# Optimization experiments

Measured on AMD Instinct MI355X. Metric: run time of the kernel, lower is better.

The kernel has to match this reference:

```python
import jax, jax.numpy as jnp
import numpy as np

H = 64           # edge/node/global hidden size
IN_F = 4         # node_attr_size
OUT_F = 1        # out_size
NUM_EMB = 100    # edge_num_embeddings
SKIP = True


def setup_inputs() -> dict:
    key = jax.random.key(0)
    ks = jax.random.split(key, 24)
    T, N, E = 4, 20000, 320000
    NNZ = 340000
    inp = {
        'node_attr': jax.random.normal(ks[0], (T, N, IN_F), jnp.float32),
        'global_attr': jax.random.normal(ks[1], (1, H), jnp.float32),
        'L_values': jax.random.normal(ks[2], (NNZ,), jnp.float32),
        'coeff': jnp.ones((1,), jnp.float32),
        'edge_attr': jax.random.randint(ks[3], (T, E), 0, NUM_EMB),
        'edge_index': jax.random.randint(ks[4], (2, E), 0, N),
        'L_index': jax.random.randint(ks[5], (2, NNZ), 0, N),
        'num_processing_steps': 4,
        # parameters
        'emb': jax.random.normal(ks[6], (NUM_EMB, H), jnp.float32) * 0.05,
        'W_ne': jax.random.normal(ks[7], (IN_F, H), jnp.float32) * 0.1,
        'b_ne': jnp.zeros((H,), jnp.float32),
        'W_eb': jax.random.normal(ks[8], ((H + 2 * H) * 2 + H, H), jnp.float32) * 0.05,
        'b_eb': jnp.zeros((H,), jnp.float32),
        'W_nb': jax.random.normal(ks[9], (2 * H + 2 * H + H, H), jnp.float32) * 0.05,
        'b_nb': jnp.zeros((H,), jnp.float32),
        'W_gb': jax.random.normal(ks[10], (H + H + H, H), jnp.float32) * 0.05,
        'b_gb': jnp.zeros((H,), jnp.float32),
        'W_d1': jax.random.normal(ks[11], (H, H), jnp.float32) * 0.1,
        'b_d1': jnp.zeros((H,), jnp.float32),
        'W_d2': jax.random.normal(ks[12], (H, OUT_F), jnp.float32) * 0.1,
        'b_d2': jnp.zeros((OUT_F,), jnp.float32),
        'W_i1': jax.random.normal(ks[13], (H, H), jnp.float32) * 0.1,
        'b_i1': jnp.zeros((H,), jnp.float32),
        'W_i2': jax.random.normal(ks[14], (H, IN_F), jnp.float32) * 0.1,
        'b_i2': jnp.zeros((IN_F,), jnp.float32),
    }
    return inp


def reference(node_attr, global_attr, L_values, coeff, emb, W_ne, b_ne,
              W_eb, b_eb, W_nb, b_nb, W_gb, b_gb, W_d1, b_d1, W_d2, b_d2,
              W_i1, b_i1, W_i2, b_i2, edge_attr, edge_index, L_index,
              num_processing_steps):
    T, N, _ = node_attr.shape
    s, r = edge_index[0], edge_index[1]
    Li, Lj = L_index[0], L_index[1]

    # encoders (all T steps at once)
    x_enc = jax.nn.relu(node_attr @ W_ne + b_ne)   # [T,N,H]
    e_enc = emb[edge_attr]                         # [T,E,H]

    def laplacian(h):  # sparse sp_L @ h, h: [N,H]
        return jax.ops.segment_sum(L_values[:, None] * h[Lj], Li, num_segments=N)

    def step(carry, xe):
        h_x, h_e, h_g = carry
        x_t, e_t = xe
        node_cat = jnp.concatenate([x_t, h_x], axis=-1)          # [N,2H]
        edge_cat = jnp.concatenate([e_t, h_e], axis=-1)          # [E,2H]
        g = h_g[0]                                               # [H]
        E_ = edge_cat.shape[0]
        # EdgeBlock: edges + sender + receiver + globals
        eb_in = jnp.concatenate([edge_cat, node_cat[s], node_cat[r],
                                 jnp.broadcast_to(g, (E_, g.shape[0]))], axis=-1)
        e_new = jax.nn.relu(eb_in @ W_eb + b_eb)                 # [E,H]
        # NodeBlock: scatter_add aggregates of received/sent edges
        recv = jax.ops.segment_sum(e_new, r, num_segments=N)
        sent = jax.ops.segment_sum(e_new, s, num_segments=N)
        nb_in = jnp.concatenate([recv, sent, node_cat,
                                 jnp.broadcast_to(g, (N, g.shape[0]))], axis=-1)
        x_new = jax.nn.relu(nb_in @ W_nb + b_nb)                 # [N,H]
        # GlobalBlock: scatter_mean (single graph -> mean)
        gb_in = jnp.concatenate([e_new.mean(0), x_new.mean(0), g])[None]
        g_new = jax.nn.relu(gb_in @ W_gb + b_gb)                 # [1,H]
        h_x_next = h_x + x_new if SKIP else x_new
        time_d = h_x_next - h_x
        spat_d = coeff[0] * laplacian(h_x_next)  # pde='diff': coeff * L u
        return (h_x_next, e_new, g_new), (h_x_next, time_d, spat_d)

    h0 = (jnp.zeros((N, H), jnp.float32),
          jnp.zeros((e_enc.shape[1], H), jnp.float32),
          global_attr)
    _, (hid, time_d, spat_d) = jax.lax.scan(step, h0, (x_enc, e_enc))

    # decoders over all steps
    out_nodes = jax.nn.relu(hid @ W_d1 + b_d1) @ W_d2 + b_d2     # [T,N,OUT_F]
    pred_in = jax.nn.relu(hid @ W_i1 + b_i1) @ W_i2 + b_i2       # [T,N,IN_F]
    return out_nodes, time_d, spat_d, pred_in
```

## Files before the change

kernel.cpp:

```cpp
#include <hip/hip_runtime.h>

#define TT 4
#define NN 20000
#define EE 320000
#define NZ 340000

typedef __attribute__((ext_vector_type(8))) __bf16 bf16x8;
typedef __attribute__((ext_vector_type(16))) float f32x16;

__device__ __forceinline__ unsigned short f2bf(float f) {
    unsigned int u = __float_as_uint(f);
    u = (u + 0x7FFFu + ((u >> 16) & 1u)) >> 16;
    return (unsigned short)u;
}
__device__ __forceinline__ float bf2f(unsigned short h) {
    return __uint_as_float(((unsigned int)h) << 16);
}

#define GLL16(src, dst) __builtin_amdgcn_global_load_lds( \
    (const __attribute__((address_space(1))) unsigned int*)(src), \
    (__attribute__((address_space(3))) unsigned int*)(dst), 16, 0, 0)

__global__ void k_count(const int* __restrict__ r, const int* __restrict__ s,
                        const int* __restrict__ Li,
                        int* cnt_r, int* cnt_s, int* cnt_L) {
    int i = blockIdx.x * 256 + threadIdx.x;
    if (i < EE) { atomicAdd(&cnt_r[r[i]], 1); atomicAdd(&cnt_s[s[i]], 1); }
    if (i < NZ) { atomicAdd(&cnt_L[Li[i]], 1); }
}

__global__ __launch_bounds__(1024) void k_scan(int* cnt, int* rowp, int* wp) {
    int which = blockIdx.x;
    int* c = cnt + which * NN;
    int* row = rowp + which * (NN + 1);
    int* w = wp + which * NN;
    __shared__ int ssum[1024];
    int tid = threadIdx.x;
    const int CH = (NN + 1023) / 1024;
    int base = tid * CH;
    int s = 0;
    for (int i = 0; i < CH; ++i) { int idx = base + i; s += (idx < NN) ? c[idx] : 0; }
    ssum[tid] = s;
    __syncthreads();
    for (int o = 1; o < 1024; o <<= 1) {
        int v = (tid >= o) ? ssum[tid - o] : 0;
        __syncthreads();
        ssum[tid] += v;
        __syncthreads();
    }
    int run = (tid > 0) ? ssum[tid - 1] : 0;
    for (int i = 0; i < CH; ++i) {
        int idx = base + i;
        if (idx < NN) { row[idx] = run; w[idx] = run; run += c[idx]; }
    }
    if (tid == 1023) row[NN] = ssum[1023];
}

__global__ void k_scatter(const int* __restrict__ r, const int* __restrict__ s,
                          const int* __restrict__ Li, const int* __restrict__ Lj,
                          const float* __restrict__ Lv,
                          int* wp_r, int* wp_s, int* wp_L,
                          int* col_r, int* col_s, int* col_Lj, float* col_Lv) {
    int i = blockIdx.x * 256 + threadIdx.x;
    if (i < EE) {
        col_r[atomicAdd(&wp_r[r[i]], 1)] = i;
        col_s[atomicAdd(&wp_s[s[i]], 1)] = i;
    }
    if (i < NZ) {
        int pos = atomicAdd(&wp_L[Li[i]], 1);
        col_Lj[pos] = Lj[i];
        col_Lv[pos] = Lv[i];
    }
}

__global__ __launch_bounds__(256) void k_pack(
    const float* __restrict__ W_eb, const float* __restrict__ W_nb,
    const float* __restrict__ W_d1, const float* __restrict__ W_i1,
    const float* __restrict__ emb, unsigned short* __restrict__ Bpe,
    unsigned short* __restrict__ Bpn, unsigned short* __restrict__ Bpd,
    unsigned short* __restrict__ emb_bf) {
    int t = blockIdx.x * 256 + threadIdx.x;
    if (t < 2 * 24 * 512) {
        int i = t & 7, l = (t >> 3) & 63, kb = (t >> 9) % 24, ch = t / (24 * 512);
        int colv = ch * 32 + (l & 31);
        int k = kb * 16 + (l >> 5) * 8 + i;
        Bpe[t] = f2bf(W_eb[k * 64 + colv]);
    }
    if (t < 2 * 16 * 512) {
        int i = t & 7, l = (t >> 3) & 63, kb = (t >> 9) % 16, ch = t / (16 * 512);
        int colv = ch * 32 + (l & 31);
        int k = kb * 16 + (l >> 5) * 8 + i;
        Bpn[t] = f2bf(W_nb[k * 64 + colv]);
    }
    if (t < 4 * 4 * 512) {
        int i = t & 7, l = (t >> 3) & 63, kb = (t >> 9) & 3, sec = t >> 11;
        int colv = (sec & 1) * 32 + (l & 31);
        int k = kb * 16 + (l >> 5) * 8 + i;
        const float* W = (sec < 2) ? W_d1 : W_i1;
        Bpd[t] = f2bf(W[k * 64 + colv]);
    }
    if (t < 100 * 64) emb_bf[t] = f2bf(emb[t]);
}

__global__ __launch_bounds__(256) void k_xenc(const float* __restrict__ na,
                                              const float* __restrict__ W_ne,
                                              const float* __restrict__ b_ne,
                                              unsigned short* __restrict__ xenc) {
    int row = blockIdx.x * 4 + (threadIdx.x >> 6);
    int j = threadIdx.x & 63;
    float4 a = *(const float4*)&na[(size_t)row * 4];
    float v = b_ne[j] + a.x * W_ne[j] + a.y * W_ne[64 + j] + a.z * W_ne[128 + j] + a.w * W_ne[192 + j];
    xenc[(size_t)row * 64 + j] = f2bf(fmaxf(v, 0.f));
}

__global__ void k_gbias(int do_update, const float* __restrict__ W_gb,
                        const float* __restrict__ b_gb, const float* __restrict__ W_eb,
                        const float* __restrict__ b_eb, const float* __restrict__ W_nb,
                        const float* __restrict__ b_nb, float* __restrict__ g_cur,
                        float* __restrict__ e_sum, float* __restrict__ x_sum,
                        float* __restrict__ gb_eb, float* __restrict__ gb_nb) {
    int j = threadIdx.x;
    float a = 0.f;
    if (do_update) {
        a = b_gb[j];
        for (int k = 0; k < 64; ++k) a += (e_sum[k] / (float)EE) * W_gb[k * 64 + j];
        for (int k = 0; k < 64; ++k) a += (x_sum[k] / (float)NN) * W_gb[(64 + k) * 64 + j];
        for (int k = 0; k < 64; ++k) a += g_cur[k] * W_gb[(128 + k) * 64 + j];
    }
    __syncthreads();
    if (do_update) {
        g_cur[j] = fmaxf(a, 0.f);
        e_sum[j] = 0.f;
        x_sum[j] = 0.f;
    }
    __syncthreads();
    float a1 = b_eb[j], a2 = b_nb[j];
    for (int k = 0; k < 64; ++k) {
        float gk = g_cur[k];
        a1 = fmaf(gk, W_eb[(384 + k) * 64 + j], a1);
        a2 = fmaf(gk, W_nb[(256 + k) * 64 + j], a2);
    }
    gb_eb[j] = a1;
    gb_nb[j] = a2;
}

__global__ __launch_bounds__(512) void k_edge(
    const unsigned short* __restrict__ xenc_t, unsigned short* __restrict__ h_e,
    const unsigned short* __restrict__ hx_bf, const unsigned short* __restrict__ emb_bf,
    const int* __restrict__ eattr_t, const int* __restrict__ sidx,
    const int* __restrict__ ridx, const unsigned short* __restrict__ Bp,
    const float* __restrict__ gbias, float* __restrict__ e_sum) {
    __shared__ unsigned short sBe[24576];
    __shared__ float sRed[8][64];
    const int tid = threadIdx.x;
    const int w = tid >> 6, ln = tid & 63;
    const int er = ln & 31, hi = ln >> 5;
    const int ebase = blockIdx.x * 256 + w * 32;
    const int e = ebase + er;
    const int si = sidx[e], ri = ridx[e], ai = eattr_t[e];

    #pragma unroll
    for (int i = 0; i < 6; ++i) {
        int off = i * 4096 + w * 512;
        GLL16(Bp + off + ln * 8, sBe + off);
    }

    const unsigned short* base0 = emb_bf + (size_t)64 * ai + hi * 8;
    const unsigned short* base1 = h_e + (size_t)64 * e + hi * 8;
    const unsigned short* base2 = xenc_t + (size_t)64 * si + hi * 8;
    const unsigned short* base3 = hx_bf + (size_t)64 * si + hi * 8;
    const unsigned short* base4 = xenc_t + (size_t)64 * ri + hi * 8;
    const unsigned short* base5 = hx_bf + (size_t)64 * ri + hi * 8;
    const unsigned short* bases[6] = {base0, base1, base2, base3, base4, base5};

    f32x16 acc0, acc1;
    #pragma unroll
    for (int i = 0; i < 16; ++i) { acc0[i] = 0.f; acc1[i] = 0.f; }

    bf16x8 c0 = *(const bf16x8*)(base0);
    bf16x8 c1 = *(const bf16x8*)(base0 + 16);
    bf16x8 c2 = *(const bf16x8*)(base0 + 32);
    bf16x8 c3 = *(const bf16x8*)(base0 + 48);

    __syncthreads();

    #pragma unroll
    for (int c = 0; c < 6; ++c) {
        bf16x8 n0, n1, n2, n3;
        if (c < 5) {
            const unsigned short* nb = bases[c + 1];
            n0 = *(const bf16x8*)(nb);
            n1 = *(const bf16x8*)(nb + 16);
            n2 = *(const bf16x8*)(nb + 32);
            n3 = *(const bf16x8*)(nb + 48);
        }
        {
            bf16x8 b0 = *(const bf16x8*)&sBe[((c * 4 + 0) * 64 + ln) * 8];
            bf16x8 b1 = *(const bf16x8*)&sBe[((24 + c * 4 + 0) * 64 + ln) * 8];
            acc0 = __builtin_amdgcn_mfma_f32_32x32x16_bf16(c0, b0, acc0, 0, 0, 0);
            acc1 = __builtin_amdgcn_mfma_f32_32x32x16_bf16(c0, b1, acc1, 0, 0, 0);
            b0 = *(const bf16x8*)&sBe[((c * 4 + 1) * 64 + ln) * 8];
            b1 = *(const bf16x8*)&sBe[((24 + c * 4 + 1) * 64 + ln) * 8];
            acc0 = __builtin_amdgcn_mfma_f32_32x32x16_bf16(c1, b0, acc0, 0, 0, 0);
            acc1 = __builtin_amdgcn_mfma_f32_32x32x16_bf16(c1, b1, acc1, 0, 0, 0);
            b0 = *(const bf16x8*)&sBe[((c * 4 + 2) * 64 + ln) * 8];
            b1 = *(const bf16x8*)&sBe[((24 + c * 4 + 2) * 64 + ln) * 8];
            acc0 = __builtin_amdgcn_mfma_f32_32x32x16_bf16(c2, b0, acc0, 0, 0, 0);
            acc1 = __builtin_amdgcn_mfma_f32_32x32x16_bf16(c2, b1, acc1, 0, 0, 0);
            b0 = *(const bf16x8*)&sBe[((c * 4 + 3) * 64 + ln) * 8];
            b1 = *(const bf16x8*)&sBe[((24 + c * 4 + 3) * 64 + ln) * 8];
            acc0 = __builtin_amdgcn_mfma_f32_32x32x16_bf16(c3, b0, acc0, 0, 0, 0);
            acc1 = __builtin_amdgcn_mfma_f32_32x32x16_bf16(c3, b1, acc1, 0, 0, 0);
        }
        c0 = n0; c1 = n1; c2 = n2; c3 = n3;
    }

    const float gb0 = gbias[er], gb1 = gbias[er + 32];
    float cs0 = 0.f, cs1 = 0.f;
    #pragma unroll
    for (int r = 0; r < 16; ++r) {
        int row = (r & 3) + 8 * (r >> 2) + 4 * hi;
        size_t o = (size_t)(ebase + row) * 64;
        float v0 = fmaxf(acc0[r] + gb0, 0.f);
        float v1 = fmaxf(acc1[r] + gb1, 0.f);
        cs0 += v0; cs1 += v1;
        h_e[o + er] = f2bf(v0);
        h_e[o + er + 32] = f2bf(v1);
    }
    cs0 += __shfl_xor(cs0, 32, 64);
    cs1 += __shfl_xor(cs1, 32, 64);
    if (hi == 0) { sRed[w][er] = cs0; sRed[w][er + 32] = cs1; }
    __syncthreads();
    if (w == 0) {
        float t = 0.f;
        #pragma unroll
        for (int q = 0; q < 8; ++q) t += sRed[q][ln];
        atomicAdd(&e_sum[ln], t);
    }
}

__global__ __launch_bounds__(256) void k_gather(
    const unsigned short* __restrict__ h_e, const int* __restrict__ row_r,
    const int* __restrict__ col_r, const int* __restrict__ row_s,
    const int* __restrict__ col_s, unsigned short* __restrict__ recv,
    unsigned short* __restrict__ sentb) {
    int t = blockIdx.x * 256 + threadIdx.x;
    int g = t & 15, n = t >> 4;
    float a0, a1, a2, a3;
    uint2 packed;

    a0 = a1 = a2 = a3 = 0.f;
    int b0 = row_r[n], b1 = row_r[n + 1];
    for (int p = b0; p < b1; ++p) {
        uint2 v = *(const uint2*)&h_e[(size_t)64 * col_r[p] + g * 4];
        a0 += bf2f((unsigned short)(v.x & 0xFFFF));
        a1 += bf2f((unsigned short)(v.x >> 16));
        a2 += bf2f((unsigned short)(v.y & 0xFFFF));
        a3 += bf2f((unsigned short)(v.y >> 16));
    }
    packed.x = (unsigned int)f2bf(a0) | ((unsigned int)f2bf(a1) << 16);
    packed.y = (unsigned int)f2bf(a2) | ((unsigned int)f2bf(a3) << 16);
    *(uint2*)&recv[(size_t)64 * n + g * 4] = packed;

    a0 = a1 = a2 = a3 = 0.f;
    b0 = row_s[n]; b1 = row_s[n + 1];
    for (int p = b0; p < b1; ++p) {
        uint2 v = *(const uint2*)&h_e[(size_t)64 * col_s[p] + g * 4];
        a0 += bf2f((unsigned short)(v.x & 0xFFFF));
        a1 += bf2f((unsigned short)(v.x >> 16));
        a2 += bf2f((unsigned short)(v.y & 0xFFFF));
        a3 += bf2f((unsigned short)(v.y >> 16));
    }
    packed.x = (unsigned int)f2bf(a0) | ((unsigned int)f2bf(a1) << 16);
    packed.y = (unsigned int)f2bf(a2) | ((unsigned int)f2bf(a3) << 16);
    *(uint2*)&sentb[(size_t)64 * n + g * 4] = packed;
}

#define NODE_CHUNK(CIDX, BASE)                                                          \
    {                                                                                   \
        const unsigned short* src = (BASE) + hi * 8;                                    \
        _Pragma("unroll") for (int kb = 0; kb < 4; ++kb) {                              \
            bf16x8 a = *(const bf16x8*)(src + kb * 16);                                 \
            bf16x8 b0 = *(const bf16x8*)&Bp[(size_t)(((CIDX)*4 + kb) * 64 + ln) * 8];   \
            bf16x8 b1 = *(const bf16x8*)&Bp[(size_t)((16 + (CIDX)*4 + kb) * 64 + ln) * 8]; \
            acc0 = __builtin_amdgcn_mfma_f32_32x32x16_bf16(a, b0, acc0, 0, 0, 0);       \
            acc1 = __builtin_amdgcn_mfma_f32_32x32x16_bf16(a, b1, acc1, 0, 0, 0);       \
        }                                                                               \
    }

__global__ __launch_bounds__(64) void k_node(
    const unsigned short* __restrict__ recv, const unsigned short* __restrict__ sentb,
    const unsigned short* __restrict__ xenc_t, float* __restrict__ h_x,
    unsigned short* __restrict__ hx_bf, const unsigned short* __restrict__ Bp,
    const float* __restrict__ gbias, float* __restrict__ x_sum,
    unsigned short* __restrict__ hid_t, float* __restrict__ timed_t) {
    const int ln = threadIdx.x;
    const int er = ln & 31, hi = ln >> 5;
    const int n0 = blockIdx.x * 32;
    const int n = n0 + er;

    f32x16 acc0, acc1;
    #pragma unroll
    for (int i = 0; i < 16; ++i) { acc0[i] = 0.f; acc1[i] = 0.f; }

    NODE_CHUNK(0, recv + (size_t)64 * n)
    NODE_CHUNK(1, sentb + (size_t)64 * n)
    NODE_CHUNK(2, xenc_t + (size_t)64 * n)
    NODE_CHUNK(3, hx_bf + (size_t)64 * n)

    const float gb0 = gbias[er], gb1 = gbias[er + 32];
    float cs0 = 0.f, cs1 = 0.f;
    #pragma unroll
    for (int r = 0; r < 16; ++r) {
        int row = (r & 3) + 8 * (r >> 2) + 4 * hi;
        size_t o = (size_t)(n0 + row) * 64;
        float x0 = fmaxf(acc0[r] + gb0, 0.f);
        float x1 = fmaxf(acc1[r] + gb1, 0.f);
        cs0 += x0; cs1 += x1;
        float hx0 = h_x[o + er] + x0;
        float hx1 = h_x[o + er + 32] + x1;
        unsigned short hb0 = f2bf(hx0), hb1 = f2bf(hx1);
        h_x[o + er] = hx0;        h_x[o + er + 32] = hx1;
        hx_bf[o + er] = hb0;      hx_bf[o + er + 32] = hb1;
        hid_t[o + er] = hb0;      hid_t[o + er + 32] = hb1;
        timed_t[o + er] = x0;     timed_t[o + er + 32] = x1;
    }
    cs0 += __shfl_xor(cs0, 32, 64);
    cs1 += __shfl_xor(cs1, 32, 64);
    if (hi == 0) {
        atomicAdd(&x_sum[er], cs0);
        atomicAdd(&x_sum[er + 32], cs1);
    }
}

__global__ __launch_bounds__(256) void k_lap(
    const float* __restrict__ h_x, const int* __restrict__ row_L,
    const int* __restrict__ col_Lj, const float* __restrict__ col_Lv,
    const float* __restrict__ coeff, float* __restrict__ spat_t) {
    int t = blockIdx.x * 256 + threadIdx.x;
    int g = t & 15, n = t >> 4;
    float a0 = 0.f, a1 = 0.f, a2 = 0.f, a3 = 0.f;
    int b0 = row_L[n], b1 = row_L[n + 1];
    for (int p = b0; p < b1; ++p) {
        float lv = col_Lv[p];
        int j = col_Lj[p];
        float4 v = *(const float4*)&h_x[(size_t)64 * j + g * 4];
        a0 = fmaf(lv, v.x, a0);
        a1 = fmaf(lv, v.y, a1);
        a2 = fmaf(lv, v.z, a2);
        a3 = fmaf(lv, v.w, a3);
    }
    float c = coeff[0];
    float4 outv = {c * a0, c * a1, c * a2, c * a3};
    *(float4*)&spat_t[(size_t)64 * n + g * 4] = outv;
}

__global__ __launch_bounds__(256) void k_dec(
    const unsigned short* __restrict__ hid_bf, const unsigned short* __restrict__ Bpd,
    const float* __restrict__ b_d1, const float* __restrict__ W_d2,
    const float* __restrict__ b_d2, const float* __restrict__ b_i1,
    const float* __restrict__ W_i2, const float* __restrict__ b_i2,
    float* __restrict__ out_nodes, float* __restrict__ pred_in) {
    __shared__ unsigned short sDec[4][32 * 138];
    const int tid = threadIdx.x;
    const int w = tid >> 6, ln = tid & 63;
    const int er = ln & 31, hi = ln >> 5;
    const int row0 = (blockIdx.x * 4 + w) * 32;

    f32x16 ad0, ad1, ai0, ai1;
    #pragma unroll
    for (int i = 0; i < 16; ++i) { ad0[i] = 0.f; ad1[i] = 0.f; ai0[i] = 0.f; ai1[i] = 0.f; }

    const unsigned short* src = hid_bf + (size_t)(row0 + er) * 64 + hi * 8;
    #pragma unroll
    for (int kb = 0; kb < 4; ++kb) {
        bf16x8 a = *(const bf16x8*)(src + kb * 16);
        bf16x8 bd0 = *(const bf16x8*)&Bpd[((0 * 4 + kb) * 64 + ln) * 8];
        bf16x8 bd1 = *(const bf16x8*)&Bpd[((4 + kb) * 64 + ln) * 8];
        bf16x8 bi0 = *(const bf16x8*)&Bpd[((8 + kb) * 64 + ln) * 8];
        bf16x8 bi1 = *(const bf16x8*)&Bpd[((12 + kb) * 64 + ln) * 8];
        ad0 = __builtin_amdgcn_mfma_f32_32x32x16_bf16(a, bd0, ad0, 0, 0, 0);
        ad1 = __builtin_amdgcn_mfma_f32_32x32x16_bf16(a, bd1, ad1, 0, 0, 0);
        ai0 = __builtin_amdgcn_mfma_f32_32x32x16_bf16(a, bi0, ai0, 0, 0, 0);
        ai1 = __builtin_amdgcn_mfma_f32_32x32x16_bf16(a, bi1, ai1, 0, 0, 0);
    }

    const float bd0v = b_d1[er], bd1v = b_d1[er + 32];
    const float bi0v = b_i1[er], bi1v = b_i1[er + 32];
    unsigned short* sw = &sDec[w][0];
    #pragma unroll
    for (int r = 0; r < 16; ++r) {
        int row = (r & 3) + 8 * (r >> 2) + 4 * hi;
        sw[row * 138 + er]       = f2bf(fmaxf(ad0[r] + bd0v, 0.f));
        sw[row * 138 + er + 32]  = f2bf(fmaxf(ad1[r] + bd1v, 0.f));
        sw[row * 138 + er + 64]  = f2bf(fmaxf(ai0[r] + bi0v, 0.f));
        sw[row * 138 + er + 96]  = f2bf(fmaxf(ai1[r] + bi1v, 0.f));
    }
    __syncthreads();

    const int g_row = row0 + er;
    if (hi == 0) {
        float s = 0.f;
        for (int k = 0; k < 32; ++k) {
            unsigned int u = *(const unsigned int*)&sw[er * 138 + 2 * k];
            s = fmaf(bf2f((unsigned short)(u & 0xFFFF)), W_d2[2 * k], s);
            s = fmaf(bf2f((unsigned short)(u >> 16)), W_d2[2 * k + 1], s);
        }
        out_nodes[g_row] = s + b_d2[0];
    } else {
        float s0 = 0.f, s1 = 0.f, s2 = 0.f, s3 = 0.f;
        for (int k = 0; k < 32; ++k) {
            unsigned int u = *(const unsigned int*)&sw[er * 138 + 64 + 2 * k];
            float vlo = bf2f((unsigned short)(u & 0xFFFF));
            float vhi = bf2f((unsigned short)(u >> 16));
            float4 w0 = *(const float4*)&W_i2[(2 * k) * 4];
            float4 w1 = *(const float4*)&W_i2[(2 * k + 1) * 4];
            s0 = fmaf(vlo, w0.x, fmaf(vhi, w1.x, s0));
            s1 = fmaf(vlo, w0.y, fmaf(vhi, w1.y, s1));
            s2 = fmaf(vlo, w0.z, fmaf(vhi, w1.z, s2));
            s3 = fmaf(vlo, w0.w, fmaf(vhi, w1.w, s3));
        }
        float4 pv = {s0 + b_i2[0], s1 + b_i2[1], s2 + b_i2[2], s3 + b_i2[3]};
        *(float4*)&pred_in[(size_t)4 * g_row] = pv;
    }
}

extern "C" void kernel_launch(void* const* d_in, const int* in_sizes, int n_in,
                              void* d_out, int out_size, void* d_ws, size_t ws_size,
                              hipStream_t stream) {
    (void)in_sizes; (void)n_in; (void)out_size; (void)ws_size;
    const float* node_attr   = (const float*)d_in[0];
    const float* global_attr = (const float*)d_in[1];
    const float* L_values    = (const float*)d_in[2];
    const float* coeff       = (const float*)d_in[3];
    const int*   edge_attr   = (const int*)d_in[4];
    const int*   edge_index  = (const int*)d_in[5];
    const int*   L_index     = (const int*)d_in[6];
    const float* emb  = (const float*)d_in[8];
    const float* W_ne = (const float*)d_in[9];
    const float* b_ne = (const float*)d_in[10];
    const float* W_eb = (const float*)d_in[11];
    const float* b_eb = (const float*)d_in[12];
    const float* W_nb = (const float*)d_in[13];
    const float* b_nb = (const float*)d_in[14];
    const float* W_gb = (const float*)d_in[15];
    const float* b_gb = (const float*)d_in[16];
    const float* W_d1 = (const float*)d_in[17];
    const float* b_d1 = (const float*)d_in[18];
    const float* W_d2 = (const float*)d_in[19];
    const float* b_d2 = (const float*)d_in[20];
    const float* W_i1 = (const float*)d_in[21];
    const float* b_i1 = (const float*)d_in[22];
    const float* W_i2 = (const float*)d_in[23];
    const float* b_i2 = (const float*)d_in[24];

    const int* s_idx = edge_index;
    const int* r_idx = edge_index + EE;
    const int* Li = L_index;
    const int* Lj = L_index + NZ;

    char* ws = (char*)d_ws;
    size_t off = 0;
    auto alloc = [&](size_t bytes) -> void* {
        void* p = ws + off;
        off = (off + bytes + 255) & ~(size_t)255;
        return p;
    };
    unsigned short* xenc   = (unsigned short*)alloc((size_t)TT * NN * 64 * 2);
    unsigned short* hid    = (unsigned short*)alloc((size_t)TT * NN * 64 * 2);
    float*          h_x    = (float*)alloc((size_t)NN * 64 * 4);
    unsigned short* hx_bf  = (unsigned short*)alloc((size_t)NN * 64 * 2);
    unsigned short* h_e    = (unsigned short*)alloc((size_t)EE * 64 * 2);
    unsigned short* recv   = (unsigned short*)alloc((size_t)NN * 64 * 2);
    unsigned short* sentb  = (unsigned short*)alloc((size_t)NN * 64 * 2);
    float* smalls          = (float*)alloc(2048);
    unsigned short* Bpe    = (unsigned short*)alloc((size_t)2 * 24 * 512 * 2);
    unsigned short* Bpn    = (unsigned short*)alloc((size_t)2 * 16 * 512 * 2);
    unsigned short* Bpd    = (unsigned short*)alloc((size_t)4 * 4 * 512 * 2);
    unsigned short* emb_bf = (unsigned short*)alloc((size_t)100 * 64 * 2);
    int* cnt    = (int*)alloc((size_t)3 * NN * 4);
    int* rowp   = (int*)alloc((size_t)3 * (NN + 1) * 4);
    int* wp     = (int*)alloc((size_t)3 * NN * 4);
    int* col_r  = (int*)alloc((size_t)EE * 4);
    int* col_s  = (int*)alloc((size_t)EE * 4);
    int* col_Lj = (int*)alloc((size_t)NZ * 4);
    float* col_Lv = (float*)alloc((size_t)NZ * 4);

    float* g_cur = smalls;
    float* e_sum = smalls + 64;
    float* x_sum = smalls + 128;
    float* gb_eb = smalls + 192;
    float* gb_nb = smalls + 256;
    int* cnt_r = cnt, *cnt_s = cnt + NN, *cnt_L = cnt + 2 * NN;
    int* row_r = rowp, *row_s = rowp + (NN + 1), *row_L = rowp + 2 * (NN + 1);
    int* wp_r = wp, *wp_s = wp + NN, *wp_L = wp + 2 * NN;

    float* out_nodes = (float*)d_out;
    float* time_d = out_nodes + (size_t)TT * NN;
    float* spat_d = time_d + (size_t)TT * NN * 64;
    float* pred_in = spat_d + (size_t)TT * NN * 64;

    hipMemsetAsync(h_x, 0, (size_t)NN * 64 * 4, stream);
    hipMemsetAsync(hx_bf, 0, (size_t)NN * 64 * 2, stream);
    hipMemsetAsync(h_e, 0, (size_t)EE * 64 * 2, stream);
    hipMemsetAsync(smalls, 0, 2048, stream);
    hipMemsetAsync(cnt, 0, (size_t)3 * NN * 4, stream);
    hipMemcpyAsync(g_cur, global_attr, 64 * 4, hipMemcpyDeviceToDevice, stream);

    k_count<<<(NZ + 255) / 256, 256, 0, stream>>>(r_idx, s_idx, Li, cnt_r, cnt_s, cnt_L);
    k_scan<<<3, 1024, 0, stream>>>(cnt, rowp, wp);
    k_scatter<<<(NZ + 255) / 256, 256, 0, stream>>>(r_idx, s_idx, Li, Lj, L_values,
                                                    wp_r, wp_s, wp_L,
                                                    col_r, col_s, col_Lj, col_Lv);
    k_pack<<<96, 256, 0, stream>>>(W_eb, W_nb, W_d1, W_i1, emb, Bpe, Bpn, Bpd, emb_bf);
    k_xenc<<<TT * NN / 4, 256, 0, stream>>>(node_attr, W_ne, b_ne, xenc);
    k_gbias<<<1, 64, 0, stream>>>(0, W_gb, b_gb, W_eb, b_eb, W_nb, b_nb,
                                  g_cur, e_sum, x_sum, gb_eb, gb_nb);

    for (int t = 0; t < TT; ++t) {
        const unsigned short* xenc_t = xenc + (size_t)t * NN * 64;
        k_edge<<<EE / 256, 512, 0, stream>>>(xenc_t, h_e, hx_bf, emb_bf,
                                             edge_attr + (size_t)t * EE, s_idx, r_idx,
                                             Bpe, gb_eb, e_sum);
        k_gather<<<NN * 16 / 256, 256, 0, stream>>>(h_e, row_r, col_r, row_s, col_s,
                                                    recv, sentb);
        k_node<<<NN / 32, 64, 0, stream>>>(recv, sentb, xenc_t, h_x, hx_bf,
                                           Bpn, gb_nb, x_sum,
                                           hid + (size_t)t * NN * 64,
                                           time_d + (size_t)t * NN * 64);
        k_lap<<<NN * 16 / 256, 256, 0, stream>>>(h_x, row_L, col_Lj, col_Lv, coeff,
                                                 spat_d + (size_t)t * NN * 64);
        k_gbias<<<1, 64, 0, stream>>>(1, W_gb, b_gb, W_eb, b_eb, W_nb, b_nb,
                                      g_cur, e_sum, x_sum, gb_eb, gb_nb);
    }
    k_dec<<<TT * NN / 128, 256, 0, stream>>>(hid, Bpd, b_d1, W_d2, b_d2,
                                             b_i1, W_i2, b_i2, out_nodes, pred_in);
}
```

Measured before the change: 761.8 us.

## Precompute per-node sender/receiver edge projections and split gather/laplacian work across threads

```diff
diff --git a/kernel.cpp b/kernel.cpp
--- a/kernel.cpp
+++ b/kernel.cpp
@@ -60,7 +60,7 @@
                           const int* __restrict__ Li, const int* __restrict__ Lj,
                           const float* __restrict__ Lv,
                           int* wp_r, int* wp_s, int* wp_L,
-                          int* col_r, int* col_s, int* col_Lj, float* col_Lv) {
+                          int* col_r, int* col_s, uint2* col_L8) {
     int i = blockIdx.x * 256 + threadIdx.x;
     if (i < EE) {
         col_r[atomicAdd(&wp_r[r[i]], 1)] = i;
@@ -68,8 +68,10 @@
     }
     if (i < NZ) {
         int pos = atomicAdd(&wp_L[Li[i]], 1);
-        col_Lj[pos] = Lj[i];
-        col_Lv[pos] = Lv[i];
+        uint2 v;
+        v.x = (unsigned int)Lj[i];
+        v.y = __float_as_uint(Lv[i]);
+        col_L8[pos] = v;
     }
 }
 
@@ -77,14 +79,20 @@
     const float* __restrict__ W_eb, const float* __restrict__ W_nb,
     const float* __restrict__ W_d1, const float* __restrict__ W_i1,
     const float* __restrict__ emb, unsigned short* __restrict__ Bpe,
-    unsigned short* __restrict__ Bpn, unsigned short* __restrict__ Bpd,
-    unsigned short* __restrict__ emb_bf) {
+    unsigned short* __restrict__ Bpu, unsigned short* __restrict__ Bpn,
+    unsigned short* __restrict__ Bpd, unsigned short* __restrict__ emb_bf) {
     int t = blockIdx.x * 256 + threadIdx.x;
-    if (t < 2 * 24 * 512) {
-        int i = t & 7, l = (t >> 3) & 63, kb = (t >> 9) % 24, ch = t / (24 * 512);
+    if (t < 2 * 8 * 512) {
+        int i = t & 7, l = (t >> 3) & 63, kb = (t >> 9) & 7, ch = t >> 12;
         int colv = ch * 32 + (l & 31);
         int k = kb * 16 + (l >> 5) * 8 + i;
         Bpe[t] = f2bf(W_eb[k * 64 + colv]);
+    }
+    if (t < 4 * 8 * 512) {
+        int i = t & 7, l = (t >> 3) & 63, kb = (t >> 9) & 7, g = t >> 12;
+        int colv = (g & 1) * 32 + (l & 31);
+        int k = 128 + (g >> 1) * 128 + kb * 16 + (l >> 5) * 8 + i;
+        Bpu[t] = f2bf(W_eb[k * 64 + colv]);
     }
     if (t < 2 * 16 * 512) {
         int i = t & 7, l = (t >> 3) & 63, kb = (t >> 9) % 16, ch = t / (16 * 512);
@@ -144,85 +152,112 @@
     gb_nb[j] = a2;
 }
 
+__global__ __launch_bounds__(64) void k_usr(
+    const unsigned short* __restrict__ xenc_t, const unsigned short* __restrict__ hx_bf,
+    const unsigned short* __restrict__ Bpu, float2* __restrict__ usr) {
+    const int ln = threadIdx.x;
+    const int er = ln & 31, hi = ln >> 5;
+    const int n0 = blockIdx.x * 32;
+    const int n = n0 + er;
+
+    f32x16 a0, a1, a2, a3;
+    #pragma unroll
+    for (int i = 0; i < 16; ++i) { a0[i] = 0.f; a1[i] = 0.f; a2[i] = 0.f; a3[i] = 0.f; }
+
+    const unsigned short* sx = xenc_t + (size_t)64 * n + hi * 8;
+    const unsigned short* sh = hx_bf + (size_t)64 * n + hi * 8;
+    #pragma unroll
+    for (int c = 0; c < 2; ++c) {
+        const unsigned short* src = c ? sh : sx;
+        #pragma unroll
+        for (int kb = 0; kb < 4; ++kb) {
+            bf16x8 a = *(const bf16x8*)(src + kb * 16);
+            int kg = c * 4 + kb;
+            bf16x8 b0 = *(const bf16x8*)&Bpu[(size_t)((0 * 8 + kg) * 64 + ln) * 8];
+            bf16x8 b1 = *(const bf16x8*)&Bpu[(size_t)((1 * 8 + kg) * 64 + ln) * 8];
+            bf16x8 b2 = *(const bf16x8*)&Bpu[(size_t)((2 * 8 + kg) * 64 + ln) * 8];
+            bf16x8 b3 = *(const bf16x8*)&Bpu[(size_t)((3 * 8 + kg) * 64 + ln) * 8];
+            a0 = __builtin_amdgcn_mfma_f32_32x32x16_bf16(a, b0, a0, 0, 0, 0);
+            a1 = __builtin_amdgcn_mfma_f32_32x32x16_bf16(a, b1, a1, 0, 0, 0);
+            a2 = __builtin_amdgcn_mfma_f32_32x32x16_bf16(a, b2, a2, 0, 0, 0);
+            a3 = __builtin_amdgcn_mfma_f32_32x32x16_bf16(a, b3, a3, 0, 0, 0);
+        }
+    }
+    #pragma unroll
+    for (int r = 0; r < 16; ++r) {
+        int row = (r & 3) + 8 * (r >> 2) + 4 * hi;
+        size_t o = (size_t)(n0 + row) * 64;
+        float2 vs = {a0[r], a1[r]};
+        float2 vr = {a2[r], a3[r]};
+        usr[o + er] = vs;
+        usr[o + 32 + er] = vr;
+    }
+}
+
 __global__ __launch_bounds__(512) void k_edge(
-    const unsigned short* __restrict__ xenc_t, unsigned short* __restrict__ h_e,
-    const unsigned short* __restrict__ hx_bf, const unsigned short* __restrict__ emb_bf,
-    const int* __restrict__ eattr_t, const int* __restrict__ sidx,
-    const int* __restrict__ ridx, const unsigned short* __restrict__ Bp,
-    const float* __restrict__ gbias, float* __restrict__ e_sum) {
-    __shared__ unsigned short sBe[24576];
+    unsigned short* __restrict__ h_e, const unsigned short* __restrict__ emb_bf,
+    const float2* __restrict__ usr, const int* __restrict__ eattr_t,
+    const int* __restrict__ sidx, const int* __restrict__ ridx,
+    const unsigned short* __restrict__ Bp, const float* __restrict__ gbias,
+    float* __restrict__ e_sum) {
+    __shared__ unsigned short sBe[8192];
     __shared__ float sRed[8][64];
     const int tid = threadIdx.x;
     const int w = tid >> 6, ln = tid & 63;
     const int er = ln & 31, hi = ln >> 5;
     const int ebase = blockIdx.x * 256 + w * 32;
     const int e = ebase + er;
-    const int si = sidx[e], ri = ridx[e], ai = eattr_t[e];
-
-    #pragma unroll
-    for (int i = 0; i < 6; ++i) {
+
+    const int siv = sidx[ebase + er];
+    const int riv = ridx[ebase + er];
+    const int ai = eattr_t[e];
+
+    #pragma unroll
+    for (int i = 0; i < 2; ++i) {
         int off = i * 4096 + w * 512;
         GLL16(Bp + off + ln * 8, sBe + off);
     }
 
-    const unsigned short* base0 = emb_bf + (size_t)64 * ai + hi * 8;
-    const unsigned short* base1 = h_e + (size_t)64 * e + hi * 8;
-    const unsigned short* base2 = xenc_t + (size_t)64 * si + hi * 8;
-    const unsigned short* base3 = hx_bf + (size_t)64 * si + hi * 8;
-    const unsigned short* base4 = xenc_t + (size_t)64 * ri + hi * 8;
-    const unsigned short* base5 = hx_bf + (size_t)64 * ri + hi * 8;
-    const unsigned short* bases[6] = {base0, base1, base2, base3, base4, base5};
+    const unsigned short* s0 = emb_bf + (size_t)64 * ai + hi * 8;
+    const unsigned short* s1 = h_e + (size_t)64 * e + hi * 8;
+    bf16x8 a0 = *(const bf16x8*)(s0);
+    bf16x8 a1 = *(const bf16x8*)(s0 + 16);
+    bf16x8 a2 = *(const bf16x8*)(s0 + 32);
+    bf16x8 a3 = *(const bf16x8*)(s0 + 48);
+    bf16x8 a4 = *(const bf16x8*)(s1);
+    bf16x8 a5 = *(const bf16x8*)(s1 + 16);
+    bf16x8 a6 = *(const bf16x8*)(s1 + 32);
+    bf16x8 a7 = *(const bf16x8*)(s1 + 48);
 
     f32x16 acc0, acc1;
     #pragma unroll
     for (int i = 0; i < 16; ++i) { acc0[i] = 0.f; acc1[i] = 0.f; }
 
-    bf16x8 c0 = *(const bf16x8*)(base0);
-    bf16x8 c1 = *(const bf16x8*)(base0 + 16);
-    bf16x8 c2 = *(const bf16x8*)(base0 + 32);
-    bf16x8 c3 = *(const bf16x8*)(base0 + 48);
-
     __syncthreads();
 
-    #pragma unroll
-    for (int c = 0; c < 6; ++c) {
-        bf16x8 n0, n1, n2, n3;
-        if (c < 5) {
-            const unsigned short* nb = bases[c + 1];
-            n0 = *(const bf16x8*)(nb);
-            n1 = *(const bf16x8*)(nb + 16);
-            n2 = *(const bf16x8*)(nb + 32);
-            n3 = *(const bf16x8*)(nb + 48);
+    #define EMM(AF, KG)                                                              \
+        {                                                                            \
+            bf16x8 b0 = *(const bf16x8*)&sBe[(((KG)) * 64 + ln) * 8];                \
+            bf16x8 b1 = *(const bf16x8*)&sBe[((8 + (KG)) * 64 + ln) * 8];            \
+            acc0 = __builtin_amdgcn_mfma_f32_32x32x16_bf16(AF, b0, acc0, 0, 0, 0);   \
+            acc1 = __builtin_amdgcn_mfma_f32_32x32x16_bf16(AF, b1, acc1, 0, 0, 0);   \
         }
-        {
-            bf16x8 b0 = *(const bf16x8*)&sBe[((c * 4 + 0) * 64 + ln) * 8];
-            bf16x8 b1 = *(const bf16x8*)&sBe[((24 + c * 4 + 0) * 64 + ln) * 8];
-            acc0 = __builtin_amdgcn_mfma_f32_32x32x16_bf16(c0, b0, acc0, 0, 0, 0);
-            acc1 = __builtin_amdgcn_mfma_f32_32x32x16_bf16(c0, b1, acc1, 0, 0, 0);
-            b0 = *(const bf16x8*)&sBe[((c * 4 + 1) * 64 + ln) * 8];
-            b1 = *(const bf16x8*)&sBe[((24 + c * 4 + 1) * 64 + ln) * 8];
-            acc0 = __builtin_amdgcn_mfma_f32_32x32x16_bf16(c1, b0, acc0, 0, 0, 0);
-            acc1 = __builtin_amdgcn_mfma_f32_32x32x16_bf16(c1, b1, acc1, 0, 0, 0);
-            b0 = *(const bf16x8*)&sBe[((c * 4 + 2) * 64 + ln) * 8];
-            b1 = *(const bf16x8*)&sBe[((24 + c * 4 + 2) * 64 + ln) * 8];
-            acc0 = __builtin_amdgcn_mfma_f32_32x32x16_bf16(c2, b0, acc0, 0, 0, 0);
-            acc1 = __builtin_amdgcn_mfma_f32_32x32x16_bf16(c2, b1, acc1, 0, 0, 0);
-            b0 = *(const bf16x8*)&sBe[((c * 4 + 3) * 64 + ln) * 8];
-            b1 = *(const bf16x8*)&sBe[((24 + c * 4 + 3) * 64 + ln) * 8];
-            acc0 = __builtin_amdgcn_mfma_f32_32x32x16_bf16(c3, b0, acc0, 0, 0, 0);
-            acc1 = __builtin_amdgcn_mfma_f32_32x32x16_bf16(c3, b1, acc1, 0, 0, 0);
-        }
-        c0 = n0; c1 = n1; c2 = n2; c3 = n3;
-    }
+    EMM(a0, 0) EMM(a1, 1) EMM(a2, 2) EMM(a3, 3)
+    EMM(a4, 4) EMM(a5, 5) EMM(a6, 6) EMM(a7, 7)
+    #undef EMM
 
     const float gb0 = gbias[er], gb1 = gbias[er + 32];
     float cs0 = 0.f, cs1 = 0.f;
     #pragma unroll
     for (int r = 0; r < 16; ++r) {
         int row = (r & 3) + 8 * (r >> 2) + 4 * hi;
+        int si_row = __shfl(siv, row, 64);
+        int ri_row = __shfl(riv, row, 64);
+        float2 us = usr[(size_t)si_row * 64 + er];
+        float2 ur = usr[(size_t)ri_row * 64 + 32 + er];
         size_t o = (size_t)(ebase + row) * 64;
-        float v0 = fmaxf(acc0[r] + gb0, 0.f);
-        float v1 = fmaxf(acc1[r] + gb1, 0.f);
+        float v0 = fmaxf(acc0[r] + us.x + ur.x + gb0, 0.f);
+        float v1 = fmaxf(acc1[r] + us.y + ur.y + gb1, 0.f);
         cs0 += v0; cs1 += v1;
         h_e[o + er] = f2bf(v0);
         h_e[o + er + 32] = f2bf(v1);
@@ -245,35 +280,25 @@
     const int* __restrict__ col_s, unsigned short* __restrict__ recv,
     unsigned short* __restrict__ sentb) {
     int t = blockIdx.x * 256 + threadIdx.x;
-    int g = t & 15, n = t >> 4;
-    float a0, a1, a2, a3;
-    uint2 packed;
-
-    a0 = a1 = a2 = a3 = 0.f;
-    int b0 = row_r[n], b1 = row_r[n + 1];
+    int sub = t & 31, n = t >> 5;
+    int g = sub & 15, which = sub >> 4;
+    const int* rowp = which ? row_s : row_r;
+    const int* colp = which ? col_s : col_r;
+    unsigned short* outp = which ? sentb : recv;
+
+    float a0 = 0.f, a1 = 0.f, a2 = 0.f, a3 = 0.f;
+    int b0 = rowp[n], b1 = rowp[n + 1];
     for (int p = b0; p < b1; ++p) {
-        uint2 v = *(const uint2*)&h_e[(size_t)64 * col_r[p] + g * 4];
+        uint2 v = *(const uint2*)&h_e[(size_t)64 * colp[p] + g * 4];
         a0 += bf2f((unsigned short)(v.x & 0xFFFF));
         a1 += bf2f((unsigned short)(v.x >> 16));
         a2 += bf2f((unsigned short)(v.y & 0xFFFF));
         a3 += bf2f((unsigned short)(v.y >> 16));
     }
+    uint2 packed;
     packed.x = (unsigned int)f2bf(a0) | ((unsigned int)f2bf(a1) << 16);
     packed.y = (unsigned int)f2bf(a2) | ((unsigned int)f2bf(a3) << 16);
-    *(uint2*)&recv[(size_t)64 * n + g * 4] = packed;
-
-    a0 = a1 = a2 = a3 = 0.f;
-    b0 = row_s[n]; b1 = row_s[n + 1];
-    for (int p = b0; p < b1; ++p) {
-        uint2 v = *(const uint2*)&h_e[(size_t)64 * col_s[p] + g * 4];
-        a0 += bf2f((unsigned short)(v.x & 0xFFFF));
-        a1 += bf2f((unsigned short)(v.x >> 16));
-        a2 += bf2f((unsigned short)(v.y & 0xFFFF));
-        a3 += bf2f((unsigned short)(v.y >> 16));
-    }
-    packed.x = (unsigned int)f2bf(a0) | ((unsigned int)f2bf(a1) << 16);
-    packed.y = (unsigned int)f2bf(a2) | ((unsigned int)f2bf(a3) << 16);
-    *(uint2*)&sentb[(size_t)64 * n + g * 4] = packed;
+    *(uint2*)&outp[(size_t)64 * n + g * 4] = packed;
 }
 
 #define NODE_CHUNK(CIDX, BASE)                                                          \
@@ -335,24 +360,34 @@
 
 __global__ __launch_bounds__(256) void k_lap(
     const float* __restrict__ h_x, const int* __restrict__ row_L,
-    const int* __restrict__ col_Lj, const float* __restrict__ col_Lv,
-    const float* __restrict__ coeff, float* __restrict__ spat_t) {
+    const uint2* __restrict__ col_L8, const float* __restrict__ coeff,
+    float* __restrict__ spat_t) {
     int t = blockIdx.x * 256 + threadIdx.x;
-    int g = t & 15, n = t >> 4;
+    int sub = t & 31, n = t >> 5;
+    int g = sub & 15, half = sub >> 4;
     float a0 = 0.f, a1 = 0.f, a2 = 0.f, a3 = 0.f;
     int b0 = row_L[n], b1 = row_L[n + 1];
-    for (int p = b0; p < b1; ++p) {
-        float lv = col_Lv[p];
-        int j = col_Lj[p];
-        float4 v = *(const float4*)&h_x[(size_t)64 * j + g * 4];
+    int mid = b0 + ((b1 - b0) >> 1);
+    int p0 = half ? mid : b0;
+    int p1 = half ? b1 : mid;
+    for (int p = p0; p < p1; ++p) {
+        uint2 e = col_L8[p];
+        float lv = __uint_as_float(e.y);
+        float4 v = *(const float4*)&h_x[(size_t)64 * e.x + g * 4];
         a0 = fmaf(lv, v.x, a0);
         a1 = fmaf(lv, v.y, a1);
         a2 = fmaf(lv, v.z, a2);
         a3 = fmaf(lv, v.w, a3);
     }
-    float c = coeff[0];
-    float4 outv = {c * a0, c * a1, c * a2, c * a3};
-    *(float4*)&spat_t[(size_t)64 * n + g * 4] = outv;
+    a0 += __shfl_xor(a0, 16, 64);
+    a1 += __shfl_xor(a1, 16, 64);
+    a2 += __shfl_xor(a2, 16, 64);
+    a3 += __shfl_xor(a3, 16, 64);
+    if (half == 0) {
+        float c = coeff[0];
+        float4 outv = {c * a0, c * a1, c * a2, c * a3};
+        *(float4*)&spat_t[(size_t)64 * n + g * 4] = outv;
+    }
 }
 
 __global__ __launch_bounds__(256) void k_dec(
@@ -473,8 +508,10 @@
     unsigned short* h_e    = (unsigned short*)alloc((size_t)EE * 64 * 2);
     unsigned short* recv   = (unsigned short*)alloc((size_t)NN * 64 * 2);
     unsigned short* sentb  = (unsigned short*)alloc((size_t)NN * 64 * 2);
+    float2*         usr    = (float2*)alloc((size_t)NN * 64 * 8);
     float* smalls          = (float*)alloc(2048);
-    unsigned short* Bpe    = (unsigned short*)alloc((size_t)2 * 24 * 512 * 2);
+    unsigned short* Bpe    = (unsigned short*)alloc((size_t)2 * 8 * 512 * 2);
+    unsigned short* Bpu    = (unsigned short*)alloc((size_t)4 * 8 * 512 * 2);
     unsigned short* Bpn    = (unsigned short*)alloc((size_t)2 * 16 * 512 * 2);
     unsigned short* Bpd    = (unsigned short*)alloc((size_t)4 * 4 * 512 * 2);
     unsigned short* emb_bf = (unsigned short*)alloc((size_t)100 * 64 * 2);
@@ -483,8 +520,7 @@
     int* wp     = (int*)alloc((size_t)3 * NN * 4);
     int* col_r  = (int*)alloc((size_t)EE * 4);
     int* col_s  = (int*)alloc((size_t)EE * 4);
-    int* col_Lj = (int*)alloc((size_t)NZ * 4);
-    float* col_Lv = (float*)alloc((size_t)NZ * 4);
+    uint2* col_L8 = (uint2*)alloc((size_t)NZ * 8);
 
     float* g_cur = smalls;
     float* e_sum = smalls + 64;
@@ -511,24 +547,26 @@
     k_scan<<<3, 1024, 0, stream>>>(cnt, rowp, wp);
     k_scatter<<<(NZ + 255) / 256, 256, 0, stream>>>(r_idx, s_idx, Li, Lj, L_values,
                                                     wp_r, wp_s, wp_L,
-                                                    col_r, col_s, col_Lj, col_Lv);
-    k_pack<<<96, 256, 0, stream>>>(W_eb, W_nb, W_d1, W_i1, emb, Bpe, Bpn, Bpd, emb_bf);
+                                                    col_r, col_s, col_L8);
+    k_pack<<<96, 256, 0, stream>>>(W_eb, W_nb, W_d1, W_i1, emb,
+                                   Bpe, Bpu, Bpn, Bpd, emb_bf);
     k_xenc<<<TT * NN / 4, 256, 0, stream>>>(node_attr, W_ne, b_ne, xenc);
     k_gbias<<<1, 64, 0, stream>>>(0, W_gb, b_gb, W_eb, b_eb, W_nb, b_nb,
                                   g_cur, e_sum, x_sum, gb_eb, gb_nb);
 
     for (int t = 0; t < TT; ++t) {
         const unsigned short* xenc_t = xenc + (size_t)t * NN * 64;
-        k_edge<<<EE / 256, 512, 0, stream>>>(xenc_t, h_e, hx_bf, emb_bf,
+        k_usr<<<NN / 32, 64, 0, stream>>>(xenc_t, hx_bf, Bpu, usr);
+        k_edge<<<EE / 256, 512, 0, stream>>>(h_e, emb_bf, usr,
                                              edge_attr + (size_t)t * EE, s_idx, r_idx,
                                              Bpe, gb_eb, e_sum);
-        k_gather<<<NN * 16 / 256, 256, 0, stream>>>(h_e, row_r, col_r, row_s, col_s,
+        k_gather<<<NN * 32 / 256, 256, 0, stream>>>(h_e, row_r, col_r, row_s, col_s,
                                                     recv, sentb);
         k_node<<<NN / 32, 64, 0, stream>>>(recv, sentb, xenc_t, h_x, hx_bf,
                                            Bpn, gb_nb, x_sum,
                                            hid + (size_t)t * NN * 64,
                                            time_d + (size_t)t * NN * 64);
-        k_lap<<<NN * 16 / 256, 256, 0, stream>>>(h_x, row_L, col_Lj, col_Lv, coeff,
+        k_lap<<<NN * 32 / 256, 256, 0, stream>>>(h_x, row_L, col_L8, coeff,
                                                  spat_d + (size_t)t * NN * 64);
         k_gbias<<<1, 64, 0, stream>>>(1, W_gb, b_gb, W_eb, b_eb, W_nb, b_nb,
                                       g_cur, e_sum, x_sum, gb_eb, gb_nb);
```

After: 755.0 us. Within noise of the previous version (-0.9%).
